# Kernel optimization log

Measured on AMD Instinct MI355X. Metric: run time of the kernel, lower is better.

Reference implementation:

```python
import jax, jax.numpy as jnp
import numpy as np

INPUT_SIZE = 695 + 2 * 406 + 84  # 1591
HIDDEN = 1024
NUM_LAYERS = 2
B, T = 8, 2048


def _make_linear(key, fan_in, fan_out, forget_bias):
    kw, kb = jax.random.split(key)
    bound = 1.0 / np.sqrt(fan_in)
    W = jax.random.uniform(kw, (fan_in, fan_out), minval=-bound, maxval=bound, dtype=jnp.float32)
    b = jax.random.uniform(kb, (fan_out,), minval=-bound, maxval=bound, dtype=jnp.float32)
    H = fan_out // 3
    b = b.at[H:2 * H].set(forget_bias)  # init_input_passthrough: forget-gate bias = 6.0
    return W, b


def setup_inputs() -> dict:
    key = jax.random.key(0)
    k1, k2, k3, k4, k5 = jax.random.split(key, 5)
    prev_actions = jax.random.uniform(k1, (B, T, 695), dtype=jnp.float32)
    states = jax.random.uniform(k2, (B, T, 812), dtype=jnp.float32)
    metadata = jax.random.uniform(k3, (B, T, 84), dtype=jnp.float32)
    W1, b1 = _make_linear(k4, INPUT_SIZE, 3 * HIDDEN, 6.0)
    W2, b2 = _make_linear(k5, HIDDEN, 3 * HIDDEN, 6.0)
    return {"prev_actions": prev_actions, "states": states, "metadata": metadata,
            "W1": W1, "b1": b1, "W2": W2, "b2": b2}


def forget_mult(f, z):
    # c_t = f_t * z_t + (1 - f_t) * c_{t-1}, c_0 = 0; parallel (log-depth) scan over time.
    a = 1.0 - f          # decay
    b = f * z            # input term
    def combine(c1, c2):
        a1, b1 = c1
        a2, b2 = c2
        return a1 * a2, a2 * b1 + b2
    _, c = jax.lax.associative_scan(combine, (a, b), axis=-2)
    return c


def qrnn_layer(x, W, b):
    y = jnp.einsum('btd,dh->bth', x, W) + b          # [B,T,3H]
    Z, Fg, O = jnp.split(y, 3, axis=-1)
    C = forget_mult(jax.nn.sigmoid(Fg), jax.nn.relu(Z))  # [B,T,H]
    out = jax.nn.sigmoid(O) * C
    return out, C[..., -1, :]


def reference(prev_actions, states, metadata, W1, b1, W2, b2):
    x = jnp.concatenate([prev_actions, states, metadata], axis=-1)  # [B,T,1591]
    hs = []
    for W, b in ((W1, b1), (W2, b2)):
        x, h_last = qrnn_layer(x, W, b)
        hs.append(h_last)
    h = jnp.stack(hs, axis=-2)  # [B, num_layers, H]
    return x, h
```

## Files before the change

### kernel.cpp

```cpp
#include <hip/hip_runtime.h>

typedef unsigned short u16;
typedef unsigned int   u32;
typedef __attribute__((ext_vector_type(8))) short bf16x8;
typedef __attribute__((ext_vector_type(16))) float f32x16;
typedef __attribute__((ext_vector_type(2))) unsigned int u32x2;

#define B_ 8
#define T_ 2048
#define M_ 16384
#define N_ 3072
#define H_ 1024
#define L_ 64
#define NC_ 32

__device__ __forceinline__ u16 f2bf(float f) {
    union { float f; unsigned u; } v; v.f = f;
    unsigned r = v.u + 0x7FFFu + ((v.u >> 16) & 1u);
    return (u16)(r >> 16);
}
__device__ __forceinline__ float bf2f(u16 s) {
    union { unsigned u; float f; } v; v.u = ((unsigned)s) << 16;
    return v.f;
}
__device__ __forceinline__ float sigm(float x) {
    return 1.f / (1.f + __expf(-x));
}

__device__ __forceinline__ void gload_lds16(const void* g, void* l) {
    __builtin_amdgcn_global_load_lds(
        (const __attribute__((address_space(1))) unsigned int*)g,
        (__attribute__((address_space(3))) unsigned int*)l,
        16, 0, 0);
}

__global__ void concat_cast(const float* __restrict__ pa, const float* __restrict__ st,
                            const float* __restrict__ md, u16* __restrict__ x) {
    const int m = blockIdx.x;
    const float* pam = pa + (size_t)m * 695;
    const float* stm = st + (size_t)m * 812;
    const float* mdm = md + (size_t)m * 84;
    u16* xm = x + (size_t)m * 1600;
    for (int d = threadIdx.x; d < 1600; d += 256) {
        float v;
        if (d < 695)       v = pam[d];
        else if (d < 1507) v = stm[d - 695];
        else if (d < 1591) v = mdm[d - 1507];
        else               v = 0.f;
        xm[d] = f2bf(v);
    }
}

__global__ void wtrans(const float* __restrict__ W, u16* __restrict__ Wt, int K, int Kp) {
    __shared__ float tile[32][33];
    const int n0 = blockIdx.x << 5;
    const int k0 = blockIdx.y << 5;
    const int tx = threadIdx.x & 31, ty = threadIdx.x >> 5;
    #pragma unroll
    for (int i = 0; i < 32; i += 8) {
        int k = k0 + ty + i;
        tile[ty + i][tx] = (k < K) ? W[(size_t)k * N_ + n0 + tx] : 0.f;
    }
    __syncthreads();
    #pragma unroll
    for (int i = 0; i < 32; i += 8) {
        int n = n0 + ty + i;
        Wt[(size_t)n * Kp + k0 + tx] = f2bf(tile[tx][ty + i]);
    }
}

__global__ __launch_bounds__(512, 1)
void gemm8p(const u16* __restrict__ A, const u16* __restrict__ Bt,
            const float* __restrict__ bias, u16* __restrict__ Y,
            int Kp, int NK, int NBN) {
    __shared__ u16 lds[65536];
    const int tid = threadIdx.x;
    const int w = tid >> 6, l = tid & 63;
    const int wm = w >> 2, wn = w & 3;

    const int cpx = gridDim.x >> 3;
    const int xg = (blockIdx.x & 7) * cpx + (blockIdx.x >> 3);
    const int bm = xg / NBN, bn = xg % NBN;
    const int brow = bm << 8, bcol = bn << 8;

    const int srow = (w << 5) + (l >> 2);
    const int gslot = (l & 3) ^ ((l >> 3) & 3);
    const u16* ga = A  + (size_t)(brow + srow) * Kp + gslot * 8;
    const u16* gb = Bt + (size_t)(bcol + srow) * Kp + gslot * 8;
    const int ldst = w << 10;

    const int flK = ((l & 31) << 5) + ((((l >> 5) ^ ((l >> 1) & 3)) & 3) << 3);
    const int abase = wm << 12;
    const int bbase = 8192 + (wn << 11);

#define STG_A(r, kt) do {                                                      \
    gload_lds16(ga + (size_t)(kt) * 32,                 &lds[((r) << 14) + ldst]);        \
    gload_lds16(ga + (size_t)(kt) * 32 + 16 * (size_t)Kp, &lds[((r) << 14) + ldst + 512]); \
} while (0)
#define STG_B(r, kt) do {                                                      \
    gload_lds16(gb + (size_t)(kt) * 32,                 &lds[((r) << 14) + 8192 + ldst]);        \
    gload_lds16(gb + (size_t)(kt) * 32 + 16 * (size_t)Kp, &lds[((r) << 14) + 8192 + ldst + 512]); \
} while (0)

    f32x16 acc[4][2] = {};

    STG_A(0, 0); STG_B(0, 0);
    STG_A(1, 1); STG_B(1, 1);
    STG_A(2, 2); STG_B(2, 2);
    asm volatile("s_waitcnt vmcnt(8)" ::: "memory");
    __builtin_amdgcn_s_barrier();
    asm volatile("" ::: "memory");

#define PH(KH, STAGECODE, WAITCODE) do {                                       \
    bf16x8 af[4], bfr[2];                                                      \
    const int fl = flK ^ ((KH) << 4);                                          \
    const int cb = cur << 14;                                                  \
    _Pragma("unroll")                                                          \
    for (int mi = 0; mi < 4; ++mi)                                             \
        af[mi] = *reinterpret_cast<const bf16x8*>(&lds[cb + abase + (mi << 10) + fl]); \
    _Pragma("unroll")                                                          \
    for (int ni = 0; ni < 2; ++ni)                                             \
        bfr[ni] = *reinterpret_cast<const bf16x8*>(&lds[cb + bbase + (ni << 10) + fl]); \
    STAGECODE;                                                                 \
    WAITCODE;                                                                  \
    __builtin_amdgcn_s_barrier();                                              \
    __builtin_amdgcn_sched_barrier(0);                                         \
    __builtin_amdgcn_s_setprio(1);                                             \
    _Pragma("unroll")                                                          \
    for (int mi = 0; mi < 4; ++mi)                                             \
        _Pragma("unroll")                                                      \
        for (int ni = 0; ni < 2; ++ni)                                         \
            acc[mi][ni] = __builtin_amdgcn_mfma_f32_32x32x16_bf16(             \
                bfr[ni], af[mi], acc[mi][ni], 0, 0, 0);                        \
    __builtin_amdgcn_s_setprio(0);                                             \
    __builtin_amdgcn_sched_barrier(0);                                         \
} while (0)

    for (int kt = 0; kt < NK; ++kt) {
        const int cur = kt & 3;
        const int nxt = (kt + 3 < NK) ? kt + 3 : kt;
        const int nb = (kt + 3) & 3;
        PH(0, { STG_A(nb, nxt); },
              { asm volatile("s_waitcnt lgkmcnt(0)" ::: "memory"); });
        PH(1, { STG_B(nb, nxt); },
              { asm volatile("s_waitcnt vmcnt(8) lgkmcnt(0)" ::: "memory"); });
    }
    asm volatile("s_waitcnt vmcnt(0)" ::: "memory");

    const int m0 = brow + wm * 128 + (l & 31);
    const int nlb = bcol + wn * 64 + ((l >> 5) << 2);
    float4 bv[2][4];
    #pragma unroll
    for (int ni = 0; ni < 2; ++ni)
        #pragma unroll
        for (int q = 0; q < 4; ++q)
            bv[ni][q] = *reinterpret_cast<const float4*>(&bias[nlb + ni * 32 + q * 8]);
    #pragma unroll
    for (int mi = 0; mi < 4; ++mi) {
        u16* yrow = Y + (size_t)(m0 + mi * 32) * N_;
        #pragma unroll
        for (int ni = 0; ni < 2; ++ni) {
            #pragma unroll
            for (int q = 0; q < 4; ++q) {
                u32x2 p;
                p.x = (u32)f2bf(acc[mi][ni][q * 4 + 0] + bv[ni][q].x) |
                      ((u32)f2bf(acc[mi][ni][q * 4 + 1] + bv[ni][q].y) << 16);
                p.y = (u32)f2bf(acc[mi][ni][q * 4 + 2] + bv[ni][q].z) |
                      ((u32)f2bf(acc[mi][ni][q * 4 + 3] + bv[ni][q].w) << 16);
                *reinterpret_cast<u32x2*>(&yrow[nlb + ni * 32 + q * 8]) = p;
            }
        }
    }
#undef PH
#undef STG_A
#undef STG_B
}

__global__ void scan_p1(const u16* __restrict__ y, float* __restrict__ aprod,
                        float* __restrict__ cend) {
    const int hb = blockIdx.x & 1;
    const int chunk = (blockIdx.x >> 1) & (NC_ - 1);
    const int b = blockIdx.x >> 6;
    const int h = (hb << 9) + (threadIdx.x << 1);
    const u16* yb = y + ((size_t)b * T_ + (size_t)chunk * L_) * N_;
    float a0 = 1.f, a1 = 1.f, c0 = 0.f, c1 = 0.f;
    #pragma unroll 4
    for (int t = 0; t < L_; ++t) {
        const u32 zz = *reinterpret_cast<const u32*>(&yb[t * N_ + h]);
        const u32 ff = *reinterpret_cast<const u32*>(&yb[t * N_ + H_ + h]);
        const float f0 = sigm(bf2f((u16)ff));
        const float f1 = sigm(bf2f((u16)(ff >> 16)));
        const float z0 = fmaxf(bf2f((u16)zz), 0.f);
        const float z1 = fmaxf(bf2f((u16)(zz >> 16)), 0.f);
        c0 = f0 * z0 + (1.f - f0) * c0;  a0 *= (1.f - f0);
        c1 = f1 * z1 + (1.f - f1) * c1;  a1 *= (1.f - f1);
    }
    const size_t idx = ((size_t)b * NC_ + chunk) * H_ + h;
    *reinterpret_cast<float2*>(&aprod[idx]) = make_float2(a0, a1);
    *reinterpret_cast<float2*>(&cend[idx])  = make_float2(c0, c1);
}

__global__ void scan_p2(const float* __restrict__ aprod, const float* __restrict__ cend,
                        float* __restrict__ cin, float* __restrict__ hout, int layer) {
    const int b = blockIdx.x >> 2;
    const int h = ((blockIdx.x & 3) << 8) + threadIdx.x;
    float c = 0.f;
    #pragma unroll
    for (int k = 0; k < NC_; ++k) {
        const size_t idx = ((size_t)b * NC_ + k) * H_ + h;
        cin[idx] = c;
        c = aprod[idx] * c + cend[idx];
    }
    hout[(size_t)(((b << 1) + layer) << 10) + h] = c;
}

__global__ void scan_p3(const u16* __restrict__ y, const float* __restrict__ cin,
                        void* __restrict__ xout, int layer) {
    const int hb = blockIdx.x & 1;
    const int chunk = (blockIdx.x >> 1) & (NC_ - 1);
    const int b = blockIdx.x >> 6;
    const int h = (hb << 9) + (threadIdx.x << 1);
    const u16* yb = y + ((size_t)b * T_ + (size_t)chunk * L_) * N_;
    const size_t cidx = ((size_t)b * NC_ + chunk) * H_ + h;
    const float2 cv = *reinterpret_cast<const float2*>(&cin[cidx]);
    float c0 = cv.x, c1 = cv.y;
    u32*    xo_bf = (u32*)xout;
    float2* xo_f  = (float2*)xout;
    const size_t obase = ((size_t)b * T_ + (size_t)chunk * L_) * H_ + h;
    #pragma unroll 4
    for (int t = 0; t < L_; ++t) {
        const u32 zz = *reinterpret_cast<const u32*>(&yb[t * N_ + h]);
        const u32 ff = *reinterpret_cast<const u32*>(&yb[t * N_ + H_ + h]);
        const u32 oo = *reinterpret_cast<const u32*>(&yb[t * N_ + 2 * H_ + h]);
        const float f0 = sigm(bf2f((u16)ff));
        const float f1 = sigm(bf2f((u16)(ff >> 16)));
        const float z0 = fmaxf(bf2f((u16)zz), 0.f);
        const float z1 = fmaxf(bf2f((u16)(zz >> 16)), 0.f);
        c0 = f0 * z0 + (1.f - f0) * c0;
        c1 = f1 * z1 + (1.f - f1) * c1;
        const float o0 = sigm(bf2f((u16)oo)) * c0;
        const float o1 = sigm(bf2f((u16)(oo >> 16))) * c1;
        const size_t oi = obase + (size_t)t * H_;
        if (layer) xo_f[oi >> 1] = make_float2(o0, o1);
        else       xo_bf[oi >> 1] = (u32)f2bf(o0) | ((u32)f2bf(o1) << 16);
    }
}

extern "C" void kernel_launch(void* const* d_in, const int* in_sizes, int n_in,
                              void* d_out, int out_size, void* d_ws, size_t ws_size,
                              hipStream_t stream) {
    const float* pa = (const float*)d_in[0];
    const float* st = (const float*)d_in[1];
    const float* md = (const float*)d_in[2];
    const float* W1 = (const float*)d_in[3];
    const float* b1 = (const float*)d_in[4];
    const float* W2 = (const float*)d_in[5];
    const float* b2 = (const float*)d_in[6];
    float* out = (float*)d_out;

    char* ws = (char*)d_ws;
    const size_t y_bytes = (size_t)M_ * N_ * 2;
    const size_t x_bytes = (size_t)M_ * 1600 * 2;
    u16* y  = (u16*)ws;
    u16* x  = (u16*)(ws + y_bytes);
    u16* Wt = (u16*)(ws + y_bytes + x_bytes);
    char* scr = ws + y_bytes + (size_t)M_ * H_ * 2;
    const size_t sarr = (size_t)B_ * NC_ * H_ * 4;
    float* aprod = (float*)scr;
    float* cend  = (float*)(scr + sarr);
    float* cin   = (float*)(scr + 2 * sarr);

    float* hout = out + (size_t)M_ * H_;

    const int grid_g = (M_ / 256) * (N_ / 256);

    concat_cast<<<M_, 256, 0, stream>>>(pa, st, md, x);
    wtrans<<<dim3(N_ / 32, 50), 256, 0, stream>>>(W1, Wt, 1591, 1600);
    gemm8p<<<grid_g, 512, 0, stream>>>(x, Wt, b1, y, 1600, 50, N_ / 256);
    scan_p1<<<B_ * NC_ * 2, 256, 0, stream>>>(y, aprod, cend);
    scan_p2<<<32, 256, 0, stream>>>(aprod, cend, cin, hout, 0);
    scan_p3<<<B_ * NC_ * 2, 256, 0, stream>>>(y, cin, x, 0);

    wtrans<<<dim3(N_ / 32, 32), 256, 0, stream>>>(W2, Wt, 1024, 1024);
    gemm8p<<<grid_g, 512, 0, stream>>>(x, Wt, b2, y, 1024, 32, N_ / 256);
    scan_p1<<<B_ * NC_ * 2, 256, 0, stream>>>(y, aprod, cend);
    scan_p2<<<32, 256, 0, stream>>>(aprod, cend, cin, hout, 1);
    scan_p3<<<B_ * NC_ * 2, 256, 0, stream>>>(y, cin, out, 1);
}
```

Before: 473.8 us.

## Switch GEMM to 16x16x32 MFMA and stage output through LDS

Replaces the 32x32x16 bf16 MFMA tiling with 16x16x32 MFMAs, changing the LDS fragment addressing and reusing B fragments loaded once per k-tile across both k-halves. The epilogue now writes bias-added bf16 results into swizzled LDS and then stores full 16-byte rows to global memory, replacing scattered 8-byte stores. The aim is coalesced output writes and a different MFMA issue pattern. It adds extra barriers and an LDS round trip in the epilogue, and raises register pressure from holding 32 accumulator fragments.

```diff
diff --git a/kernel.cpp b/kernel.cpp
--- a/kernel.cpp
+++ b/kernel.cpp
@@ -3,7 +3,7 @@
 typedef unsigned short u16;
 typedef unsigned int   u32;
 typedef __attribute__((ext_vector_type(8))) short bf16x8;
-typedef __attribute__((ext_vector_type(16))) float f32x16;
+typedef __attribute__((ext_vector_type(4))) float f32x4;
 typedef __attribute__((ext_vector_type(2))) unsigned int u32x2;
 
 #define B_ 8
@@ -89,20 +89,21 @@
     const u16* gb = Bt + (size_t)(bcol + srow) * Kp + gslot * 8;
     const int ldst = w << 10;
 
-    const int flK = ((l & 31) << 5) + ((((l >> 5) ^ ((l >> 1) & 3)) & 3) << 3);
+    const int fl = ((l & 15) << 5) + ((((l >> 4) ^ ((l >> 1) & 3)) & 3) << 3);
     const int abase = wm << 12;
     const int bbase = 8192 + (wn << 11);
 
 #define STG_A(r, kt) do {                                                      \
-    gload_lds16(ga + (size_t)(kt) * 32,                 &lds[((r) << 14) + ldst]);        \
-    gload_lds16(ga + (size_t)(kt) * 32 + 16 * (size_t)Kp, &lds[((r) << 14) + ldst + 512]); \
+    gload_lds16(ga + (size_t)(kt) * 32,                   &lds[((r) << 14) + ldst]);        \
+    gload_lds16(ga + (size_t)(kt) * 32 + 16 * (size_t)Kp, &lds[((r) << 14) + ldst + 512]);  \
 } while (0)
 #define STG_B(r, kt) do {                                                      \
-    gload_lds16(gb + (size_t)(kt) * 32,                 &lds[((r) << 14) + 8192 + ldst]);        \
+    gload_lds16(gb + (size_t)(kt) * 32,                   &lds[((r) << 14) + 8192 + ldst]);       \
     gload_lds16(gb + (size_t)(kt) * 32 + 16 * (size_t)Kp, &lds[((r) << 14) + 8192 + ldst + 512]); \
 } while (0)
 
-    f32x16 acc[4][2] = {};
+    f32x4 acc[8][4] = {};
+    bf16x8 bfr[4];
 
     STG_A(0, 0); STG_B(0, 0);
     STG_A(1, 1); STG_B(1, 1);
@@ -111,16 +112,19 @@
     __builtin_amdgcn_s_barrier();
     asm volatile("" ::: "memory");
 
-#define PH(KH, STAGECODE, WAITCODE) do {                                       \
-    bf16x8 af[4], bfr[2];                                                      \
-    const int fl = flK ^ ((KH) << 4);                                          \
+#define PH(CIH, LOADB, STAGECODE, WAITCODE) do {                               \
+    bf16x8 af[4];                                                              \
     const int cb = cur << 14;                                                  \
     _Pragma("unroll")                                                          \
     for (int mi = 0; mi < 4; ++mi)                                             \
-        af[mi] = *reinterpret_cast<const bf16x8*>(&lds[cb + abase + (mi << 10) + fl]); \
-    _Pragma("unroll")                                                          \
-    for (int ni = 0; ni < 2; ++ni)                                             \
-        bfr[ni] = *reinterpret_cast<const bf16x8*>(&lds[cb + bbase + (ni << 10) + fl]); \
+        af[mi] = *reinterpret_cast<const bf16x8*>(                             \
+            &lds[cb + abase + (((CIH) * 4 + mi) << 9) + fl]);                  \
+    if (LOADB) {                                                               \
+        _Pragma("unroll")                                                      \
+        for (int ni = 0; ni < 4; ++ni)                                         \
+            bfr[ni] = *reinterpret_cast<const bf16x8*>(                        \
+                &lds[cb + bbase + (ni << 9) + fl]);                            \
+    }                                                                          \
     STAGECODE;                                                                 \
     WAITCODE;                                                                  \
     __builtin_amdgcn_s_barrier();                                              \
@@ -129,9 +133,9 @@
     _Pragma("unroll")                                                          \
     for (int mi = 0; mi < 4; ++mi)                                             \
         _Pragma("unroll")                                                      \
-        for (int ni = 0; ni < 2; ++ni)                                         \
-            acc[mi][ni] = __builtin_amdgcn_mfma_f32_32x32x16_bf16(             \
-                bfr[ni], af[mi], acc[mi][ni], 0, 0, 0);                        \
+        for (int ni = 0; ni < 4; ++ni)                                         \
+            acc[(CIH) * 4 + mi][ni] = __builtin_amdgcn_mfma_f32_16x16x32_bf16( \
+                bfr[ni], af[mi], acc[(CIH) * 4 + mi][ni], 0, 0, 0);            \
     __builtin_amdgcn_s_setprio(0);                                             \
     __builtin_amdgcn_sched_barrier(0);                                         \
 } while (0)
@@ -140,36 +144,46 @@
         const int cur = kt & 3;
         const int nxt = (kt + 3 < NK) ? kt + 3 : kt;
         const int nb = (kt + 3) & 3;
-        PH(0, { STG_A(nb, nxt); },
-              { asm volatile("s_waitcnt lgkmcnt(0)" ::: "memory"); });
-        PH(1, { STG_B(nb, nxt); },
-              { asm volatile("s_waitcnt vmcnt(8) lgkmcnt(0)" ::: "memory"); });
-    }
+        PH(0, 1, { STG_A(nb, nxt); },
+                 { asm volatile("s_waitcnt lgkmcnt(0)" ::: "memory"); });
+        PH(1, 0, { STG_B(nb, nxt); },
+                 { asm volatile("s_waitcnt vmcnt(8) lgkmcnt(0)" ::: "memory"); });
+    }
+
     asm volatile("s_waitcnt vmcnt(0)" ::: "memory");
-
-    const int m0 = brow + wm * 128 + (l & 31);
-    const int nlb = bcol + wn * 64 + ((l >> 5) << 2);
-    float4 bv[2][4];
-    #pragma unroll
-    for (int ni = 0; ni < 2; ++ni)
+    __builtin_amdgcn_s_barrier();
+
+    const int nloc0 = (wn << 6) + ((l >> 4) << 2);
+    float4 bv4[4];
+    #pragma unroll
+    for (int nf = 0; nf < 4; ++nf)
+        bv4[nf] = *reinterpret_cast<const float4*>(&bias[bcol + nloc0 + nf * 16]);
+    #pragma unroll
+    for (int ci = 0; ci < 8; ++ci) {
+        const int mrow = (wm << 7) + ((ci >> 2) << 6) + ((ci & 3) << 4) + (l & 15);
         #pragma unroll
-        for (int q = 0; q < 4; ++q)
-            bv[ni][q] = *reinterpret_cast<const float4*>(&bias[nlb + ni * 32 + q * 8]);
-    #pragma unroll
-    for (int mi = 0; mi < 4; ++mi) {
-        u16* yrow = Y + (size_t)(m0 + mi * 32) * N_;
-        #pragma unroll
-        for (int ni = 0; ni < 2; ++ni) {
-            #pragma unroll
-            for (int q = 0; q < 4; ++q) {
-                u32x2 p;
-                p.x = (u32)f2bf(acc[mi][ni][q * 4 + 0] + bv[ni][q].x) |
-                      ((u32)f2bf(acc[mi][ni][q * 4 + 1] + bv[ni][q].y) << 16);
-                p.y = (u32)f2bf(acc[mi][ni][q * 4 + 2] + bv[ni][q].z) |
-                      ((u32)f2bf(acc[mi][ni][q * 4 + 3] + bv[ni][q].w) << 16);
-                *reinterpret_cast<u32x2*>(&yrow[nlb + ni * 32 + q * 8]) = p;
-            }
+        for (int nf = 0; nf < 4; ++nf) {
+            const int nloc = nloc0 + nf * 16;
+            u32x2 p;
+            p.x = (u32)f2bf(acc[ci][nf][0] + bv4[nf].x) |
+                  ((u32)f2bf(acc[ci][nf][1] + bv4[nf].y) << 16);
+            p.y = (u32)f2bf(acc[ci][nf][2] + bv4[nf].z) |
+                  ((u32)f2bf(acc[ci][nf][3] + bv4[nf].w) << 16);
+            const int off = (mrow << 8) + (((nloc >> 3) ^ (mrow & 7)) << 3) +
+                            ((nloc >> 2) & 1) * 4;
+            *reinterpret_cast<u32x2*>(&lds[off]) = p;
         }
+    }
+    asm volatile("s_waitcnt lgkmcnt(0)" ::: "memory");
+    __builtin_amdgcn_s_barrier();
+
+    #pragma unroll
+    for (int rp = 0; rp < 16; ++rp) {
+        const int row = (w << 5) + (rp << 1) + (l >> 5);
+        const int c16 = l & 31;
+        const bf16x8 v = *reinterpret_cast<const bf16x8*>(
+            &lds[(row << 8) + ((c16 ^ (row & 7)) << 3)]);
+        *reinterpret_cast<bf16x8*>(&Y[(size_t)(brow + row) * N_ + bcol + c16 * 8]) = v;
     }
 #undef PH
 #undef STG_A
```

Measured after the change: 431.7 us. -8.9%, faster.
